# Optimization experiments

Measured on AMD Instinct MI355X. Metric: run time of the kernel, lower is better.

## Reference

```python
import jax, jax.numpy as jnp
import numpy as np


def _ward_agglomerative(xf: np.ndarray, k: int) -> np.ndarray:
    """Ward-linkage agglomerative clustering (sklearn default), returning
    integer labels in [0, k) for each of the n rows of xf.

    Sequential Lance-Williams merge loop: this IS the algorithm's math and is
    inherently sequential (the reason this module has kernel headroom).
    Per-merge updates are fully vectorized over the n 'other' clusters.
    """
    xf = np.asarray(xf, dtype=np.float64)
    n = xf.shape[0]
    # initial squared-euclidean distances (Ward criterion on singletons)
    sq = np.sum(xf * xf, axis=1)
    d2 = sq[:, None] + sq[None, :] - 2.0 * (xf @ xf.T)
    np.maximum(d2, 0.0, out=d2)
    np.fill_diagonal(d2, np.inf)

    sizes = np.ones(n, dtype=np.float64)
    active = np.ones(n, dtype=bool)
    cluster_of = np.arange(n)  # point -> current representative cluster id
    idxs = np.arange(n)

    for _ in range(n - k):
        flat = np.argmin(d2)  # inactive rows/cols are +inf
        i, j = divmod(flat, n)
        if i > j:
            i, j = j, i
        dij = d2[i, j]
        si, sj = sizes[i], sizes[j]
        m = active.copy()
        m[i] = False
        m[j] = False
        sm = sizes[m]
        # Lance-Williams Ward update on squared distances (vectorized over m)
        new_d = ((si + sm) * d2[i, m] + (sj + sm) * d2[j, m] - sm * dij) / (si + sj + sm)
        d2[i, m] = new_d
        d2[m, i] = new_d
        sizes[i] = si + sj
        active[j] = False
        d2[j, :] = np.inf
        d2[:, j] = np.inf
        d2[i, i] = np.inf
        cluster_of[cluster_of == j] = i

    # relabel surviving cluster ids to 0..k-1 by first occurrence
    _, labels = np.unique(cluster_of, return_inverse=True)
    return labels.astype(np.int32)


def setup_inputs() -> dict:
    key = jax.random.key(0)
    x = jax.random.uniform(key, (4, 512, 96), dtype=jnp.float32)  # [B, N, D]
    return {"x": x, "num_clusters": 100}


def reference(x, num_clusters):
    # Faithful translation of HierarchicalClustering.forward:
    # flatten batch+tokens, Ward agglomerative clustering, one-hot scatter.
    B, N, D = x.shape
    xf = np.asarray(jax.device_get(x)).reshape(B * N, D)
    labels = _ward_agglomerative(xf, int(num_clusters))  # [B*N]
    onehot = jax.nn.one_hot(jnp.asarray(labels), int(num_clusters), dtype=jnp.float32)
    return onehot.reshape(B, N, int(num_clusters))
```

## Files before the change

### kernel.cpp

```cpp
#include <hip/hip_runtime.h>
#include <math.h>

#define NPTS   2048
#define DIM    96
#define PITCH  2048
#define TB     8
#define ROUNDS 48

__device__ double g_cent[DIM * PITCH];
__device__ double g_sz[NPTS];
__device__ double g_nrm[NPTS];
__device__ int    g_act[NPTS];
__device__ double g_nnv[NPTS];
__device__ int    g_nni[NPTS];
__device__ int    g_reci[NPTS];
__device__ int    g_recj[NPTS];
__device__ double g_rech[NPTS];
__device__ int    g_a, g_done, g_mcount;

__global__ void init_kernel(const float* __restrict__ x) {
    int p = blockIdx.x * 256 + threadIdx.x;
    if (p < NPTS) {
        double nr = 0.0;
        for (int d = 0; d < DIM; ++d) {
            double v = (double)x[p * DIM + d];
            g_cent[d * PITCH + p] = v;
            nr += v * v;
        }
        g_nrm[p] = nr; g_sz[p] = 1.0; g_act[p] = 1;
        g_nni[p] = -1; g_nnv[p] = (double)INFINITY;
        g_reci[p] = 0; g_recj[p] = 0; g_rech[p] = (double)INFINITY;
    }
    if (p == 0) { g_a = NPTS; g_done = 0; g_mcount = 0; }
}

__global__ void __launch_bounds__(512) nn_pass() {
    if (g_done) return;
    const int tile0 = blockIdx.x * TB;
    const int t = threadIdx.x;

    __shared__ int    sAct[TB];
    __shared__ double sMu[DIM * TB];
    __shared__ double sNb[TB], sSb[TB];
    __shared__ double sRedV[8 * TB];
    __shared__ int    sRedI[8 * TB];

    if (t < TB) {
        sAct[t] = g_act[tile0 + t];
        sNb[t]  = g_nrm[tile0 + t];
        sSb[t]  = g_sz[tile0 + t];
    }
    __syncthreads();
    int anyact = 0;
#pragma unroll
    for (int bi = 0; bi < TB; ++bi) anyact |= sAct[bi];
    if (!anyact) return;

    for (int e = t; e < DIM * TB; e += 512)
        sMu[e] = g_cent[(e >> 3) * PITCH + tile0 + (e & 7)];
    __syncthreads();

    double acc[4][TB];
#pragma unroll
    for (int q = 0; q < 4; ++q)
#pragma unroll
        for (int bi = 0; bi < TB; ++bi) acc[q][bi] = 0.0;

    for (int d = 0; d < DIM; ++d) {
        double mu[TB];
#pragma unroll
        for (int bi = 0; bi < TB; ++bi) mu[bi] = sMu[d * TB + bi];
        double x0 = g_cent[d * PITCH + t];
        double x1 = g_cent[d * PITCH + t + 512];
        double x2 = g_cent[d * PITCH + t + 1024];
        double x3 = g_cent[d * PITCH + t + 1536];
#pragma unroll
        for (int bi = 0; bi < TB; ++bi) {
            acc[0][bi] += mu[bi] * x0;
            acc[1][bi] += mu[bi] * x1;
            acc[2][bi] += mu[bi] * x2;
            acc[3][bi] += mu[bi] * x3;
        }
    }

    double bv[TB]; int bidx[TB];
#pragma unroll
    for (int bi = 0; bi < TB; ++bi) { bv[bi] = (double)INFINITY; bidx[bi] = 0x7FFFFFFF; }
#pragma unroll
    for (int q = 0; q < 4; ++q) {
        int m  = t + q * 512;
        int am = g_act[m];
        double sm = g_sz[m], nm = g_nrm[m];
#pragma unroll
        for (int bi = 0; bi < TB; ++bi) {
            int bcol = tile0 + bi;
            double f = (sSb[bi] * sm) / (sSb[bi] + sm);
            double D = (2.0 * f) * ((sNb[bi] + nm) - 2.0 * acc[q][bi]);
            if (am && m != bcol && D < bv[bi]) { bv[bi] = D; bidx[bi] = m; }
        }
    }

    const int lane = t & 63, w = t >> 6;
#pragma unroll
    for (int bi = 0; bi < TB; ++bi) {
        double v = bv[bi]; int ix = bidx[bi];
        for (int off = 1; off < 64; off <<= 1) {
            double ov = __shfl_xor(v, off);
            int    oi = __shfl_xor(ix, off);
            if (ov < v || (ov == v && oi < ix)) { v = ov; ix = oi; }
        }
        if (lane == 0) { sRedV[w * TB + bi] = v; sRedI[w * TB + bi] = ix; }
    }
    __syncthreads();
    if (t < TB && sAct[t]) {
        double v = sRedV[t]; int ix = sRedI[t];
        for (int w2 = 1; w2 < 8; ++w2) {
            double ov = sRedV[w2 * TB + t]; int oi = sRedI[w2 * TB + t];
            if (ov < v || (ov == v && oi < ix)) { v = ov; ix = oi; }
        }
        g_nnv[tile0 + t] = v;
        g_nni[tile0 + t] = ix;
    }
}

__global__ void __launch_bounds__(1024) merge_pass() {
    if (g_done) return;
    __shared__ int sNp;
    const int t = threadIdx.x;
    if (t == 0) sNp = 0;
    __syncthreads();
    for (int b = t; b < NPTS; b += 1024) {
        int j = g_nni[b];
        if (j > b && j < NPTS && g_nni[j] == b) {
            int r = atomicAdd(&g_mcount, 1);
            g_reci[r] = b; g_recj[r] = j; g_rech[r] = g_nnv[b];
            double sb = g_sz[b], sj = g_sz[j], s2 = sb + sj;
            double nr = 0.0;
            for (int d = 0; d < DIM; ++d) {
                double v = (sb * g_cent[d * PITCH + b] + sj * g_cent[d * PITCH + j]) / s2;
                g_cent[d * PITCH + b] = v;
                nr += v * v;
            }
            g_sz[b] = s2; g_nrm[b] = nr;
            g_act[j] = 0; g_nni[j] = -1; g_nnv[j] = (double)INFINITY;
            atomicAdd(&sNp, 1);
        }
    }
    __syncthreads();
    if (t == 0) {
        g_a -= sNp;
        g_done = (g_a <= 1) ? 1 : 0;
    }
}

__global__ void __launch_bounds__(1024) finisher(const int* __restrict__ kptr,
                                                 float* __restrict__ out) {
    __shared__ double D0[NPTS];
    __shared__ int    I0[NPTS];
    __shared__ int    I1[NPTS];
    __shared__ int    I2[NPTS];
    __shared__ int    I3[NPTS];
    __shared__ int    I4[NPTS];
    __shared__ int    sNp;

    const int t = threadIdx.x, lane = t & 63, w = t >> 6;
    const int k = *kptr;
    int a = g_a;

    for (int guard = 0; guard < NPTS && a > 1; ++guard) {
        for (int b = w; b < NPTS; b += 16) {
            if (!g_act[b]) { if (lane == 0) { D0[b] = (double)INFINITY; I0[b] = -1; } continue; }
            double sb = g_sz[b], nb = g_nrm[b];
            double bvv = (double)INFINITY; int bii = 0x7FFFFFFF;
            for (int m = lane; m < NPTS; m += 64) {
                if (!g_act[m] || m == b) continue;
                double dot = 0.0;
                for (int d = 0; d < DIM; ++d)
                    dot += g_cent[d * PITCH + b] * g_cent[d * PITCH + m];
                double sm = g_sz[m], nm = g_nrm[m];
                double f = (sb * sm) / (sb + sm);
                double D = (2.0 * f) * ((nb + nm) - 2.0 * dot);
                if (D < bvv || (D == bvv && m < bii)) { bvv = D; bii = m; }
            }
            for (int off = 1; off < 64; off <<= 1) {
                double ov = __shfl_xor(bvv, off);
                int    oi = __shfl_xor(bii, off);
                if (ov < bvv || (ov == bvv && oi < bii)) { bvv = ov; bii = oi; }
            }
            if (lane == 0) { D0[b] = bvv; I0[b] = bii; }
        }
        __syncthreads();
        if (t == 0) sNp = 0;
        __syncthreads();
        for (int b = t; b < NPTS; b += 1024) {
            int j = I0[b];
            if (j > b && j < NPTS && I0[j] == b) {
                int r = atomicAdd(&g_mcount, 1);
                g_reci[r] = b; g_recj[r] = j; g_rech[r] = D0[b];
                double sb = g_sz[b], sj = g_sz[j], s2 = sb + sj;
                double nr = 0.0;
                for (int d = 0; d < DIM; ++d) {
                    double v = (sb * g_cent[d * PITCH + b] + sj * g_cent[d * PITCH + j]) / s2;
                    g_cent[d * PITCH + b] = v; nr += v * v;
                }
                g_sz[b] = s2; g_nrm[b] = nr; g_act[j] = 0;
                atomicAdd(&sNp, 1);
            }
        }
        __syncthreads();
        a -= sNp;
        __syncthreads();
    }

    const int M    = g_mcount;
    const int nsel = NPTS - k;
    __syncthreads();
    for (int e = t; e < NPTS; e += 1024) {
        D0[e] = (e < M) ? g_rech[e] : (double)INFINITY;
        I0[e] = e;
    }
    __syncthreads();
    for (int k2 = 2; k2 <= NPTS; k2 <<= 1) {
        for (int j2 = k2 >> 1; j2 > 0; j2 >>= 1) {
            for (int i = t; i < NPTS; i += 1024) {
                int ixj = i ^ j2;
                if (ixj > i) {
                    bool up = ((i & k2) == 0);
                    double a0 = D0[i], a1 = D0[ixj];
                    if (up ? (a0 > a1) : (a0 < a1)) {
                        D0[i] = a1; D0[ixj] = a0;
                        int ti_ = I0[i]; I0[i] = I0[ixj]; I0[ixj] = ti_;
                    }
                }
            }
            __syncthreads();
        }
    }
    for (int p = t; p < NPTS; p += 1024) I1[p] = p;
    __syncthreads();
    for (int r = t; r < nsel; r += 1024) {
        int rec = I0[r];
        I1[g_recj[rec]] = g_reci[rec];
    }
    __syncthreads();
    int* psrc = I1; int* pdst = I2;
    for (int it2 = 0; it2 < 11; ++it2) {
        for (int p = t; p < NPTS; p += 1024) pdst[p] = psrc[psrc[p]];
        __syncthreads();
        int* tp = psrc; psrc = pdst; pdst = tp;
    }
    for (int p = t; p < NPTS; p += 1024) I3[p] = (psrc[p] == p) ? 1 : 0;
    __syncthreads();
    int* rsrc = I3; int* rdst = I4;
    for (int off = 1; off < NPTS; off <<= 1) {
        for (int p = t; p < NPTS; p += 1024)
            rdst[p] = rsrc[p] + ((p >= off) ? rsrc[p - off] : 0);
        __syncthreads();
        int* tp = rsrc; rsrc = rdst; rdst = tp;
    }
    for (int p = t; p < NPTS; p += 1024) {
        int lbl = rsrc[psrc[p]] - 1;
        out[(size_t)p * k + lbl] = 1.0f;
    }
}

extern "C" void kernel_launch(void* const* d_in, const int* in_sizes, int n_in,
                              void* d_out, int out_size, void* d_ws, size_t ws_size,
                              hipStream_t stream) {
    const float* x    = (const float*)d_in[0];
    const int*   kptr = (const int*)d_in[1];
    float*       out  = (float*)d_out;

    hipMemsetAsync(d_out, 0, (size_t)out_size * sizeof(float), stream);
    init_kernel<<<8, 256, 0, stream>>>(x);
    for (int r = 0; r < ROUNDS; ++r) {
        nn_pass<<<NPTS / TB, 512, 0, stream>>>();
        merge_pass<<<1, 1024, 0, stream>>>();
    }
    finisher<<<1, 1024, 0, stream>>>(kptr, out);
}
```

Measured before the change: 3.516 ms.

## Compact active clusters into an index list and skip inactive work in NN pass

The merge pass now builds a compacted list of active cluster indices with a wave-level prefix scan and sets the active count from it. The nearest-neighbour pass uses this list: blocks beyond the active count exit early, and centroid columns are gathered through the index list, so inactive clusters no longer cost compute or bandwidth. The price is indirect, partly uncoalesced gathers of centroid data, plus an extra scan and synchronisation in every merge pass.

New measurement: 3.475 ms. Within noise of the previous version (-1.2%).

```diff
diff --git a/kernel.cpp b/kernel.cpp
--- a/kernel.cpp
+++ b/kernel.cpp
@@ -11,6 +11,7 @@
 __device__ double g_sz[NPTS];
 __device__ double g_nrm[NPTS];
 __device__ int    g_act[NPTS];
+__device__ int    g_cidx[NPTS];
 __device__ double g_nnv[NPTS];
 __device__ int    g_nni[NPTS];
 __device__ int    g_reci[NPTS];
@@ -27,7 +28,7 @@
             g_cent[d * PITCH + p] = v;
             nr += v * v;
         }
-        g_nrm[p] = nr; g_sz[p] = 1.0; g_act[p] = 1;
+        g_nrm[p] = nr; g_sz[p] = 1.0; g_act[p] = 1; g_cidx[p] = p;
         g_nni[p] = -1; g_nnv[p] = (double)INFINITY;
         g_reci[p] = 0; g_recj[p] = 0; g_rech[p] = (double)INFINITY;
     }
@@ -36,29 +37,38 @@
 
 __global__ void __launch_bounds__(512) nn_pass() {
     if (g_done) return;
+    const int a = g_a;
     const int tile0 = blockIdx.x * TB;
+    if (tile0 >= a) return;
     const int t = threadIdx.x;
 
-    __shared__ int    sAct[TB];
+    __shared__ int    sIdx[TB];
     __shared__ double sMu[DIM * TB];
     __shared__ double sNb[TB], sSb[TB];
     __shared__ double sRedV[8 * TB];
     __shared__ int    sRedI[8 * TB];
 
     if (t < TB) {
-        sAct[t] = g_act[tile0 + t];
-        sNb[t]  = g_nrm[tile0 + t];
-        sSb[t]  = g_sz[tile0 + t];
-    }
-    __syncthreads();
-    int anyact = 0;
-#pragma unroll
-    for (int bi = 0; bi < TB; ++bi) anyact |= sAct[bi];
-    if (!anyact) return;
-
-    for (int e = t; e < DIM * TB; e += 512)
-        sMu[e] = g_cent[(e >> 3) * PITCH + tile0 + (e & 7)];
-    __syncthreads();
+        int cm   = tile0 + t;
+        int orig = (cm < a) ? g_cidx[cm] : -1;
+        sIdx[t] = orig;
+        sNb[t]  = (orig >= 0) ? g_nrm[orig] : 0.0;
+        sSb[t]  = (orig >= 0) ? g_sz[orig]  : 1.0;
+    }
+    __syncthreads();
+    for (int e = t; e < DIM * TB; e += 512) {
+        int col = sIdx[e & 7];
+        sMu[e] = (col >= 0) ? g_cent[(e >> 3) * PITCH + col] : 0.0;
+    }
+    __syncthreads();
+
+    int om[4]; bool vld[4];
+#pragma unroll
+    for (int q = 0; q < 4; ++q) {
+        int m  = t + q * 512;
+        vld[q] = (m < a);
+        om[q]  = g_cidx[vld[q] ? m : (a - 1)];
+    }
 
     double acc[4][TB];
 #pragma unroll
@@ -70,10 +80,10 @@
         double mu[TB];
 #pragma unroll
         for (int bi = 0; bi < TB; ++bi) mu[bi] = sMu[d * TB + bi];
-        double x0 = g_cent[d * PITCH + t];
-        double x1 = g_cent[d * PITCH + t + 512];
-        double x2 = g_cent[d * PITCH + t + 1024];
-        double x3 = g_cent[d * PITCH + t + 1536];
+        double x0 = g_cent[d * PITCH + om[0]];
+        double x1 = g_cent[d * PITCH + om[1]];
+        double x2 = g_cent[d * PITCH + om[2]];
+        double x3 = g_cent[d * PITCH + om[3]];
 #pragma unroll
         for (int bi = 0; bi < TB; ++bi) {
             acc[0][bi] += mu[bi] * x0;
@@ -88,15 +98,14 @@
     for (int bi = 0; bi < TB; ++bi) { bv[bi] = (double)INFINITY; bidx[bi] = 0x7FFFFFFF; }
 #pragma unroll
     for (int q = 0; q < 4; ++q) {
-        int m  = t + q * 512;
-        int am = g_act[m];
-        double sm = g_sz[m], nm = g_nrm[m];
+        if (!vld[q]) continue;
+        int    cm = t + q * 512;
+        double sm = g_sz[om[q]], nm = g_nrm[om[q]];
 #pragma unroll
         for (int bi = 0; bi < TB; ++bi) {
-            int bcol = tile0 + bi;
             double f = (sSb[bi] * sm) / (sSb[bi] + sm);
             double D = (2.0 * f) * ((sNb[bi] + nm) - 2.0 * acc[q][bi]);
-            if (am && m != bcol && D < bv[bi]) { bv[bi] = D; bidx[bi] = m; }
+            if (cm != tile0 + bi && D < bv[bi]) { bv[bi] = D; bidx[bi] = om[q]; }
         }
     }
 
@@ -112,23 +121,22 @@
         if (lane == 0) { sRedV[w * TB + bi] = v; sRedI[w * TB + bi] = ix; }
     }
     __syncthreads();
-    if (t < TB && sAct[t]) {
+    if (t < TB && tile0 + t < a) {
         double v = sRedV[t]; int ix = sRedI[t];
         for (int w2 = 1; w2 < 8; ++w2) {
             double ov = sRedV[w2 * TB + t]; int oi = sRedI[w2 * TB + t];
             if (ov < v || (ov == v && oi < ix)) { v = ov; ix = oi; }
         }
-        g_nnv[tile0 + t] = v;
-        g_nni[tile0 + t] = ix;
+        g_nnv[sIdx[t]] = v;
+        g_nni[sIdx[t]] = ix;
     }
 }
 
 __global__ void __launch_bounds__(1024) merge_pass() {
     if (g_done) return;
-    __shared__ int sNp;
-    const int t = threadIdx.x;
-    if (t == 0) sNp = 0;
-    __syncthreads();
+    __shared__ int sWave[16];
+    const int t = threadIdx.x, lane = t & 63, w = t >> 6;
+
     for (int b = t; b < NPTS; b += 1024) {
         int j = g_nni[b];
         if (j > b && j < NPTS && g_nni[j] == b) {
@@ -143,13 +151,32 @@
             }
             g_sz[b] = s2; g_nrm[b] = nr;
             g_act[j] = 0; g_nni[j] = -1; g_nnv[j] = (double)INFINITY;
-            atomicAdd(&sNp, 1);
-        }
-    }
+        }
+    }
+    __syncthreads();
+
+    int e0 = 2 * t, e1 = 2 * t + 1;
+    int c0 = g_act[e0], c1 = g_act[e1];
+    int sum = c0 + c1;
+    int v = sum;
+    for (int off = 1; off < 64; off <<= 1) {
+        int o = __shfl_up(v, off);
+        if (lane >= off) v += o;
+    }
+    if (lane == 63) sWave[w] = v;
     __syncthreads();
     if (t == 0) {
-        g_a -= sNp;
-        g_done = (g_a <= 1) ? 1 : 0;
+        int run = 0;
+        for (int i = 0; i < 16; ++i) { int x = sWave[i]; sWave[i] = run; run += x; }
+    }
+    __syncthreads();
+    int base = sWave[w] + (v - sum);
+    if (c0) g_cidx[base]      = e0;
+    if (c1) g_cidx[base + c0] = e1;
+    if (t == 1023) {
+        int a2 = base + sum;
+        g_a = a2;
+        g_done = (a2 <= 1) ? 1 : 0;
     }
 }
 
```
